# Kernel optimization log

Hardware: AMD Instinct MI355X
Metric: run time of the kernel (lower is better)

Reference implementation:

```python
import jax, jax.numpy as jnp
import numpy as np

B, K, N, E, D = 32, 32, 2048, 16384, 768
L_GNN, L_TR, H = 2, 4, 12
FF, VOCAB, N_ROLES, MAX_POS, N_HOPS = 3072, 25, 2, 64, 16


def setup_inputs() -> dict:
    key = jax.random.key(0)
    ks = jax.random.split(key, 32)
    s = 0.02
    inp = {
        "raw_features": jax.random.normal(ks[0], (B, K, D), jnp.float32),
        "x0": jax.random.randint(ks[1], (K, N), 0, VOCAB),
        "edge0": jax.random.randint(ks[2], (K, 2, E), 0, N),
        "batch0": jnp.sort(jax.random.randint(ks[3], (K, N), 0, B), axis=-1),
        "x1": jax.random.randint(ks[4], (K, N), 0, VOCAB),
        "edge1": jax.random.randint(ks[5], (K, 2, E), 0, N),
        "batch1": jnp.sort(jax.random.randint(ks[6], (K, N), 0, B), axis=-1),
        "role_ids": jax.random.randint(ks[7], (B, K), 0, N_ROLES),
        "position_ids": jax.random.randint(ks[8], (B, K), 0, MAX_POS),
        "hop_ids": jax.random.randint(ks[9], (B, K), 0, N_HOPS),
        # GNNForProtein params (shared across slots and both proteins)
        "amino_embed": jax.random.normal(ks[10], (VOCAB, D)) * s,
        "gnn_W": jax.random.normal(ks[11], (L_GNN, D, D)) * s,
        "gnn_b": jnp.zeros((L_GNN, D)),
        # GraphBert embeddings
        "role_emb": jax.random.normal(ks[12], (N_ROLES, D)) * s,
        "pos_emb": jax.random.normal(ks[13], (MAX_POS, D)) * s,
        "hop_emb": jax.random.normal(ks[14], (N_HOPS, D)) * s,
        "emb_ln_scale": jnp.ones((D,)),
        "emb_ln_bias": jnp.zeros((D,)),
        # GraphBert transformer layers (stacked over L_TR)
        "Wq": jax.random.normal(ks[15], (L_TR, D, D)) * s,
        "bq": jnp.zeros((L_TR, D)),
        "Wk": jax.random.normal(ks[16], (L_TR, D, D)) * s,
        "bk": jnp.zeros((L_TR, D)),
        "Wv": jax.random.normal(ks[17], (L_TR, D, D)) * s,
        "bv": jnp.zeros((L_TR, D)),
        "Wo": jax.random.normal(ks[18], (L_TR, D, D)) * s,
        "bo": jnp.zeros((L_TR, D)),
        "ln1_s": jnp.ones((L_TR, D)),
        "ln1_b": jnp.zeros((L_TR, D)),
        "W1": jax.random.normal(ks[19], (L_TR, D, FF)) * s,
        "b1": jnp.zeros((L_TR, FF)),
        "W2": jax.random.normal(ks[20], (L_TR, FF, D)) * s,
        "b2": jnp.zeros((L_TR, D)),
        "ln2_s": jnp.ones((L_TR, D)),
        "ln2_b": jnp.zeros((L_TR, D)),
    }
    return inp


def _ln(x, s, b):
    m = jnp.mean(x, -1, keepdims=True)
    v = jnp.mean(jnp.square(x - m), -1, keepdims=True)
    return (x - m) * jax.lax.rsqrt(v + 1e-12) * s + b


def _gnn(node_ids, edges, batch_idx, amino_embed, W, b):
    # One protein slot: GCN message passing + mean readout per graph in batch.
    h = amino_embed[node_ids]                      # [N, D]
    src, dst = edges[0], edges[1]
    for l in range(W.shape[0]):
        agg = jax.ops.segment_sum(h[src], dst, num_segments=N)
        h = jax.nn.relu((h + agg) @ W[l] + b[l])
    sums = jax.ops.segment_sum(h, batch_idx, num_segments=B)
    cnt = jax.ops.segment_sum(jnp.ones((h.shape[0], 1), h.dtype), batch_idx, num_segments=B)
    return sums / jnp.maximum(cnt, 1.0)           # [B, D]


def reference(raw_features, x0, edge0, batch0, x1, edge1, batch1, role_ids, position_ids, hop_ids,
              amino_embed, gnn_W, gnn_b, role_emb, pos_emb, hop_emb, emb_ln_scale, emb_ln_bias,
              Wq, bq, Wk, bk, Wv, bv, Wo, bo, ln1_s, ln1_b, W1, b1, W2, b2, ln2_s, ln2_b):
    # vmap over the K protein slots replaces the original Python loop (same math).
    gnn_v = jax.vmap(_gnn, in_axes=(0, 0, 0, None, None, None))
    p0 = gnn_v(x0, edge0, batch0, amino_embed, gnn_W, gnn_b)   # [K, B, D]
    p1 = gnn_v(x1, edge1, batch1, amino_embed, gnn_W, gnn_b)   # [K, B, D]
    feats = raw_features + jnp.transpose(p0 + p1, (1, 0, 2))   # [B, K, D]
    # GraphBert embeddings + encoder
    h = feats + role_emb[role_ids] + pos_emb[position_ids] + hop_emb[hop_ids]
    h = _ln(h, emb_ln_scale, emb_ln_bias)
    dh = D // H
    scale = float(1.0 / np.sqrt(dh))
    for l in range(Wq.shape[0]):
        q = (h @ Wq[l] + bq[l]).reshape(B, K, H, dh)
        kk = (h @ Wk[l] + bk[l]).reshape(B, K, H, dh)
        v = (h @ Wv[l] + bv[l]).reshape(B, K, H, dh)
        att = jax.nn.softmax(jnp.einsum('bqhd,bkhd->bhqk', q, kk) * scale, axis=-1)
        ctx = jnp.einsum('bhqk,bkhd->bqhd', att, v).reshape(B, K, D)
        h = _ln(h + ctx @ Wo[l] + bo[l], ln1_s[l], ln1_b[l])
        f = jax.nn.gelu(h @ W1[l] + b1[l]) @ W2[l] + b2[l]
        h = _ln(h + f, ln2_s[l], ln2_b[l])
    return h
```

## Files before the change

kernel.cpp:

```cpp
#include <hip/hip_runtime.h>
#include <hip/hip_bf16.h>
#include <math.h>

using bf16 = __hip_bfloat16;
typedef __attribute__((ext_vector_type(8))) short short8;
typedef __attribute__((ext_vector_type(4))) float floatx4;
typedef __attribute__((ext_vector_type(4))) short short4v;

#define NB   32
#define NK   32
#define NNODE 2048
#define NEDGE 16384
#define ND   768
#define NHH  12
#define DHH  64
#define NFF  3072
#define NG   64
#define LTR  4
#define VOCAB 25

static __device__ __forceinline__ float b2f(bf16 x) { return __bfloat162float(x); }
static __device__ __forceinline__ bf16 f2b(float x) { return __float2bfloat16(x); }
static __device__ __forceinline__ float bs2f(short s) {
    unsigned u = ((unsigned)(unsigned short)s) << 16;
    float f; __builtin_memcpy(&f, &u, 4); return f;
}
static __device__ __forceinline__ short f2bs(float x) {
    bf16 h = f2b(x); short s; __builtin_memcpy(&s, &h, 2); return s;
}

static __device__ __forceinline__ void load_lds16(const bf16* g, bf16* l) {
    __builtin_amdgcn_global_load_lds((const __attribute__((address_space(1))) void*)g,
                                     (__attribute__((address_space(3))) void*)l, 16, 0, 0);
}

static __device__ __forceinline__ float ldf(const void* p, size_t i, bool f32) {
    return f32 ? ((const float*)p)[i] : b2f(((const bf16*)p)[i]);
}

__global__ void detect_dtype_kernel(const void* __restrict__ eln_s, int* __restrict__ flag) {
    if (threadIdx.x == 0 && blockIdx.x == 0) {
        unsigned w = ((const unsigned*)eln_s)[0];
        flag[0] = (w == 0x3F800000u) ? 1 : 0;
    }
}

__device__ __forceinline__ void conv_tile(const void* __restrict__ src, size_t srcOff,
                                          bf16* __restrict__ dst, int R, int Cn,
                                          int tr, int tc, bool f32, int t,
                                          short (*tile)[70]) {
    int r0 = tr * 64, c0 = tc * 64;
    int rr = t >> 4, c4 = (t & 15) * 4;
    #pragma unroll
    for (int p = 0; p < 4; ++p) {
        int r = rr + p * 16;
        size_t base = srcOff + (size_t)(r0 + r) * Cn + c0 + c4;
        short4v s;
        if (f32) {
            float4 v = *(const float4*)((const float*)src + base);
            s.x = f2bs(v.x); s.y = f2bs(v.y); s.z = f2bs(v.z); s.w = f2bs(v.w);
        } else {
            s = *(const short4v*)((const short*)src + base);
        }
        tile[r][c4]     = s.x; tile[r][c4 + 1] = s.y;
        tile[r][c4 + 2] = s.z; tile[r][c4 + 3] = s.w;
    }
    __syncthreads();
    #pragma unroll
    for (int p = 0; p < 4; ++p) {
        int c = rr + p * 16;
        short4v o;
        o.x = tile[c4][c];     o.y = tile[c4 + 1][c];
        o.z = tile[c4 + 2][c]; o.w = tile[c4 + 3][c];
        *(short4v*)((short*)dst + (size_t)(c0 + c) * R + r0 + c4) = o;
    }
}

__global__ __launch_bounds__(256) void convert_gnn_kernel(const void* __restrict__ gnnW,
                                                          bf16* __restrict__ gnnT,
                                                          const int* __restrict__ flag) {
    __shared__ short tile[64][70];
    bool f32 = flag[0] != 0;
    int bid = blockIdx.x;
    int id = bid / 144, tl = bid % 144;
    conv_tile(gnnW, (size_t)id * 589824, gnnT + (size_t)id * 589824,
              768, 768, tl / 12, tl % 12, f32, threadIdx.x, tile);
}

__global__ __launch_bounds__(256) void convert_layer_kernel(
    const void* __restrict__ Wq, const void* __restrict__ Wk, const void* __restrict__ Wv,
    const void* __restrict__ Wo, const void* __restrict__ W1, const void* __restrict__ W2,
    int l, bf16* __restrict__ qkvT, bf16* __restrict__ oT,
    bf16* __restrict__ w1T, bf16* __restrict__ w2T, const int* __restrict__ flag) {
    __shared__ short tile[64][70];
    bool f32 = flag[0] != 0;
    int bid = blockIdx.x, t = threadIdx.x;
    if (bid < 432) {
        int m = bid / 144, tl = bid % 144;
        const void* src = (m == 0) ? Wq : ((m == 1) ? Wk : Wv);
        conv_tile(src, (size_t)l * 589824, qkvT + (size_t)m * 589824,
                  768, 768, tl / 12, tl % 12, f32, t, tile);
    } else if (bid < 576) {
        int tl = bid - 432;
        conv_tile(Wo, (size_t)l * 589824, oT, 768, 768, tl / 12, tl % 12, f32, t, tile);
    } else if (bid < 1152) {
        int tl = bid - 576;
        conv_tile(W1, (size_t)l * 768 * 3072, w1T, 768, 3072, tl / 48, tl % 48, f32, t, tile);
    } else {
        int tl = bid - 1152;
        conv_tile(W2, (size_t)l * 3072 * 768, w2T, 3072, 768, tl / 12, tl % 12, f32, t, tile);
    }
}

__global__ __launch_bounds__(256) void pack_bias_kernel(
    const void* __restrict__ gnnb, const void* __restrict__ bq, const void* __restrict__ bk,
    const void* __restrict__ bv, const void* __restrict__ bo, const void* __restrict__ b1,
    const void* __restrict__ b2, float* __restrict__ out, const int* __restrict__ flag) {
    bool f32 = flag[0] != 0;
    int i = blockIdx.x * 256 + threadIdx.x;
    if (i >= 1536 + LTR * 6912) return;
    float v;
    if (i < 1536) v = ldf(gnnb, i, f32);
    else {
        int j = i - 1536, l = j / 6912, r = j % 6912;
        if      (r <  768) v = ldf(bq, l * 768 + r, f32);
        else if (r < 1536) v = ldf(bk, l * 768 + r - 768, f32);
        else if (r < 2304) v = ldf(bv, l * 768 + r - 1536, f32);
        else if (r < 3072) v = ldf(bo, l * 768 + r - 2304, f32);
        else if (r < 6144) v = ldf(b1, l * 3072 + r - 3072, f32);
        else               v = ldf(b2, l * 768 + r - 6144, f32);
    }
    out[i] = v;
}

__global__ __launch_bounds__(192) void e1_kernel(const void* __restrict__ emb,
                                                 const bf16* __restrict__ w0T,
                                                 bf16* __restrict__ E1,
                                                 const int* __restrict__ flag) {
    bool f32 = flag[0] != 0;
    int v = blockIdx.x, t = threadIdx.x;
    float acc[4] = {0.f, 0.f, 0.f, 0.f};
    for (int k = 0; k < ND; k += 4) {
        float e0 = ldf(emb, (size_t)v * ND + k,     f32);
        float e1 = ldf(emb, (size_t)v * ND + k + 1, f32);
        float e2 = ldf(emb, (size_t)v * ND + k + 2, f32);
        float e3 = ldf(emb, (size_t)v * ND + k + 3, f32);
        #pragma unroll
        for (int j = 0; j < 4; ++j) {
            const short4v w = *(const short4v*)&w0T[(size_t)(t * 4 + j) * ND + k];
            acc[j] += e0 * bs2f(w.x) + e1 * bs2f(w.y) + e2 * bs2f(w.z) + e3 * bs2f(w.w);
        }
    }
    short4v o; o.x = f2bs(acc[0]); o.y = f2bs(acc[1]); o.z = f2bs(acc[2]); o.w = f2bs(acc[3]);
    ((short4v*)(E1 + (size_t)v * ND))[t] = o;
}

__global__ __launch_bounds__(256) void count_deg_kernel(const int* __restrict__ edge0,
                                                        const int* __restrict__ edge1,
                                                        int* __restrict__ deg) {
    int gid = blockIdx.x;
    int g = gid >> 6, chunk = gid & 63;
    const int* ep = (g < NK) ? (edge0 + (size_t)g * 2 * NEDGE)
                             : (edge1 + (size_t)(g - NK) * 2 * NEDGE);
    int e = chunk * 256 + threadIdx.x;
    int dst = ep[NEDGE + e];
    atomicAdd(&deg[g * NNODE + dst], 1);
}

__global__ __launch_bounds__(256) void scan_deg_kernel(int* __restrict__ deg,
                                                       int* __restrict__ indptr) {
    int g = blockIdx.x, t = threadIdx.x;
    __shared__ int sums[256];
    int loc[8]; int s = 0;
    #pragma unroll
    for (int i = 0; i < 8; ++i) { loc[i] = deg[g * NNODE + t * 8 + i]; s += loc[i]; }
    sums[t] = s; __syncthreads();
    for (int off = 1; off < 256; off <<= 1) {
        int v = (t >= off) ? sums[t - off] : 0;
        __syncthreads();
        sums[t] += v;
        __syncthreads();
    }
    int run = sums[t] - s;
    #pragma unroll
    for (int i = 0; i < 8; ++i) {
        indptr[g * (NNODE + 1) + t * 8 + i] = run;
        deg[g * NNODE + t * 8 + i] = run;
        run += loc[i];
    }
    if (t == 255) indptr[g * (NNODE + 1) + NNODE] = run;
}

__global__ __launch_bounds__(256) void fill_csr_kernel(const int* __restrict__ edge0,
                                                       const int* __restrict__ edge1,
                                                       int* __restrict__ cursor,
                                                       int* __restrict__ csr_src) {
    int gid = blockIdx.x;
    int g = gid >> 6, chunk = gid & 63;
    const int* ep = (g < NK) ? (edge0 + (size_t)g * 2 * NEDGE)
                             : (edge1 + (size_t)(g - NK) * 2 * NEDGE);
    int e = chunk * 256 + threadIdx.x;
    int src = ep[e];
    int dst = ep[NEDGE + e];
    int p = atomicAdd(&cursor[g * NNODE + dst], 1);
    csr_src[(size_t)g * NEDGE + p] = src;
}

__global__ __launch_bounds__(64) void batch_count_kernel(const int* __restrict__ batch0,
                                                         const int* __restrict__ batch1,
                                                         int* __restrict__ cnt) {
    int g = blockIdx.x;
    int b = threadIdx.x;
    if (b >= NB) return;
    const int* bp = (g < NK) ? (batch0 + (size_t)g * NNODE)
                             : (batch1 + (size_t)(g - NK) * NNODE);
    int lo = 0, hi = NNODE;
    while (lo < hi) { int mid = (lo + hi) >> 1; if (bp[mid] < b) lo = mid + 1; else hi = mid; }
    int start = lo;
    hi = NNODE;
    while (lo < hi) { int mid = (lo + hi) >> 1; if (bp[mid] < b + 1) lo = mid + 1; else hi = mid; }
    cnt[g * NB + b] = lo - start;
}

static __device__ __forceinline__ void node_block_decode(int id, int& gl, int& n) {
    int r = id & 7, q = id >> 3;
    gl = r + 8 * (q >> 11);
    n = q & 2047;
}

__global__ __launch_bounds__(192) void gnn_layer1_kernel(const int* __restrict__ x0,
                                                         const int* __restrict__ x1,
                                                         const bf16* __restrict__ E1,
                                                         const float* __restrict__ b0,
                                                         const int* __restrict__ indptr,
                                                         const int* __restrict__ csr_src,
                                                         bf16* __restrict__ hC, int g0) {
    int gl, n; node_block_decode(blockIdx.x, gl, n);
    int g = g0 + gl;
    const int* xg = (g < NK) ? (x0 + (size_t)g * NNODE) : (x1 + (size_t)(g - NK) * NNODE);
    int beg = indptr[g * (NNODE + 1) + n];
    int end = indptr[g * (NNODE + 1) + n + 1];
    const int* cs = csr_src + (size_t)g * NEDGE;
    int t = threadIdx.x;
    const short4v* E = (const short4v*)E1;
    short4v v = E[(size_t)xg[n] * 192 + t];
    float a0 = bs2f(v.x), a1 = bs2f(v.y), a2 = bs2f(v.z), a3 = bs2f(v.w);
    for (int e = beg; e < end; ++e) {
        int s = cs[e];
        short4v w = E[(size_t)xg[s] * 192 + t];
        a0 += bs2f(w.x); a1 += bs2f(w.y); a2 += bs2f(w.z); a3 += bs2f(w.w);
    }
    float4 bb = ((const float4*)b0)[t];
    short4v o;
    o.x = f2bs(fmaxf(a0 + bb.x, 0.f));
    o.y = f2bs(fmaxf(a1 + bb.y, 0.f));
    o.z = f2bs(fmaxf(a2 + bb.z, 0.f));
    o.w = f2bs(fmaxf(a3 + bb.w, 0.f));
    ((short4v*)(hC + ((size_t)gl * NNODE + n) * ND))[t] = o;
}

__global__ __launch_bounds__(192) void gnn_aggregate_kernel(const bf16* __restrict__ hC,
                                                            const int* __restrict__ indptr,
                                                            const int* __restrict__ csr_src,
                                                            bf16* __restrict__ xC, int g0) {
    int gl, n; node_block_decode(blockIdx.x, gl, n);
    int g = g0 + gl;
    int beg = indptr[g * (NNODE + 1) + n];
    int end = indptr[g * (NNODE + 1) + n + 1];
    const short4v* hg = (const short4v*)(hC + (size_t)gl * NNODE * ND);
    const int* cs = csr_src + (size_t)g * NEDGE;
    int t = threadIdx.x;
    short4v v = hg[(size_t)n * 192 + t];
    float a0 = bs2f(v.x), a1 = bs2f(v.y), a2 = bs2f(v.z), a3 = bs2f(v.w);
    for (int e = beg; e < end; ++e) {
        int s = cs[e];
        short4v w = hg[(size_t)s * 192 + t];
        a0 += bs2f(w.x); a1 += bs2f(w.y); a2 += bs2f(w.z); a3 += bs2f(w.w);
    }
    short4v o; o.x = f2bs(a0); o.y = f2bs(a1); o.z = f2bs(a2); o.w = f2bs(a3);
    ((short4v*)(xC + ((size_t)gl * NNODE + n) * ND))[t] = o;
}

__global__ __launch_bounds__(256) void gemm_tn(const bf16* __restrict__ A,
                                               const bf16* __restrict__ BT,
                                               const float* __restrict__ bias,
                                               void* __restrict__ C,
                                               int M, int K, int N,
                                               int act, int outF32,
                                               const int* __restrict__ batAp,
                                               const int* __restrict__ batBp,
                                               float* __restrict__ pool, int g0) {
    __shared__ bf16 lA[2][128][32];
    __shared__ bf16 lB[2][128][32];
    int nTilesN = N >> 7, nTilesM = M >> 7;
    int brow, bcol;
    if ((nTilesM & 7) == 0) {
        int xcd = blockIdx.x & 7, j = blockIdx.x >> 3;
        brow = (j / nTilesN) * 8 + xcd;
        bcol = j % nTilesN;
    } else {
        bcol = blockIdx.x % nTilesN;
        brow = blockIdx.x / nTilesN;
    }
    int t = threadIdx.x;
    int wave = t >> 6, lane = t & 63;
    int wr = wave >> 1, wc = wave & 1;
    int l15 = lane & 15, quad = lane >> 4;
    const int row0 = brow << 7, col0 = bcol << 7;
    const int sr0 = t >> 2, sk0 = (t & 3) * 8;
    const bf16* Ab = A + (size_t)(row0 + sr0) * K + sk0;
    const bf16* Bb = BT + (size_t)(col0 + sr0) * K + sk0;
    const size_t rstride = (size_t)64 * K;

    load_lds16(Ab,           &lA[0][sr0][sk0]);
    load_lds16(Ab + rstride, &lA[0][sr0 + 64][sk0]);
    load_lds16(Bb,           &lB[0][sr0][sk0]);
    load_lds16(Bb + rstride, &lB[0][sr0 + 64][sk0]);

    floatx4 acc[4][4] = {};
    int cur = 0;
    for (int k0 = 0; k0 < K; k0 += 32) {
        __syncthreads();
        if (k0 + 32 < K) {
            load_lds16(Ab + k0 + 32,           &lA[cur ^ 1][sr0][sk0]);
            load_lds16(Ab + rstride + k0 + 32, &lA[cur ^ 1][sr0 + 64][sk0]);
            load_lds16(Bb + k0 + 32,           &lB[cur ^ 1][sr0][sk0]);
            load_lds16(Bb + rstride + k0 + 32, &lB[cur ^ 1][sr0 + 64][sk0]);
        }
        short8 afr[4], bfr[4];
        #pragma unroll
        for (int i = 0; i < 4; ++i)
            afr[i] = *reinterpret_cast<const short8*>(&lA[cur][wr * 64 + i * 16 + l15][quad * 8]);
        #pragma unroll
        for (int j = 0; j < 4; ++j)
            bfr[j] = *reinterpret_cast<const short8*>(&lB[cur][wc * 64 + j * 16 + l15][quad * 8]);
        #pragma unroll
        for (int i = 0; i < 4; ++i)
            #pragma unroll
            for (int j = 0; j < 4; ++j)
                acc[i][j] = __builtin_amdgcn_mfma_f32_16x16x32_bf16(afr[i], bfr[j], acc[i][j], 0, 0, 0);
        cur ^= 1;
    }

    if (pool) {
        int g = g0 + (row0 >> 11);
        const int* bp = (g < NK) ? (batAp + (size_t)g * NNODE)
                                 : (batBp + (size_t)(g - NK) * NNODE);
        int nbase = row0 & (NNODE - 1);
        float* pg = pool + (size_t)g * NB * ND;
        int cb = wc * 64 + l15;
        float bv[4];
        #pragma unroll
        for (int j = 0; j < 4; ++j) bv[j] = bias[col0 + cb + j * 16];
        __syncthreads();
        float* lp = (float*)lA;
        int bLo = bp[nbase], bHi = bp[nbase + 127];
        int nb = (bHi - bLo + 1) * 128;
        for (int idx = t; idx < nb; idx += 256) lp[idx] = 0.f;
        __syncthreads();
        float sums[4] = {0.f, 0.f, 0.f, 0.f};
        int curb = -1;
        #pragma unroll
        for (int i = 0; i < 4; ++i) {
            int rr = nbase + wr * 64 + i * 16 + quad * 4;
            #pragma unroll
            for (int r = 0; r < 4; ++r) {
                int b = bp[rr + r];
                if (b != curb) {
                    if (curb >= 0) {
                        #pragma unroll
                        for (int j = 0; j < 4; ++j)
                            atomicAdd(&lp[(curb - bLo) * 128 + cb + j * 16], sums[j]);
                    }
                    curb = b;
                    sums[0] = sums[1] = sums[2] = sums[3] = 0.f;
                }
                #pragma unroll
                for (int j = 0; j < 4; ++j) {
                    float v = acc[i][j][r] + bv[j];
                    if (act == 1) v = fmaxf(v, 0.f);
                    sums[j] += v;
                }
            }
        }
        #pragma unroll
        for (int j = 0; j < 4; ++j)
            atomicAdd(&lp[(curb - bLo) * 128 + cb + j * 16], sums[j]);
        __syncthreads();
        for (int idx = t; idx < nb; idx += 256) {
            float v = lp[idx];
            if (v != 0.f)
                atomicAdd(&pg[(size_t)(bLo + (idx >> 7)) * ND + col0 + (idx & 127)], v);
        }
        return;
    }

    #pragma unroll
    for (int i = 0; i < 4; ++i) {
        int rbase = row0 + wr * 64 + i * 16 + quad * 4;
        #pragma unroll
        for (int j = 0; j < 4; ++j) {
            int c = col0 + wc * 64 + j * 16 + l15;
            float bv = bias[c];
            #pragma unroll
            for (int r = 0; r < 4; ++r) {
                float v = acc[i][j][r] + bv;
                if (act == 1) v = fmaxf(v, 0.f);
                else if (act == 2) {
                    float x = v;
                    float u = 1.5957691216057308f * (x + 0.044715f * x * x * x);
                    v = x / (1.f + __expf(-u));
                }
                size_t idx = (size_t)(rbase + r) * N + c;
                if (outF32) ((float*)C)[idx] = v;
                else        ((bf16*)C)[idx] = f2b(v);
            }
        }
    }
}

__global__ __launch_bounds__(256) void gemm_tn_sk(const bf16* __restrict__ A,
                                                  const bf16* __restrict__ BT,
                                                  const float* __restrict__ bias,
                                                  void* __restrict__ C,
                                                  int M, int K, int N, int splitK,
                                                  int act, int store) {
    __shared__ bf16 lA[2][64][32];
    __shared__ bf16 lB[2][128][32];
    int nTilesN = N >> 7, nTilesM = M >> 6;
    int tiles = nTilesM * nTilesN;
    int split = blockIdx.x / tiles;
    int jt = blockIdx.x % tiles;
    int brow = jt / nTilesN, bcol = jt % nTilesN;
    int t = threadIdx.x;
    int wave = t >> 6, lane = t & 63;
    int wr = wave >> 1, wc = wave & 1;
    int l15 = lane & 15, quad = lane >> 4;
    const int row0 = brow << 6, col0 = bcol << 7;
    const int kLen = K / splitK, kBeg = split * kLen;
    const int sr0 = t >> 2, sk0 = (t & 3) * 8;
    const bf16* Ab = A + (size_t)(row0 + sr0) * K + kBeg + sk0;
    const bf16* Bb = BT + (size_t)(col0 + sr0) * K + kBeg + sk0;
    const size_t rstride = (size_t)64 * K;

    load_lds16(Ab,           &lA[0][sr0][sk0]);
    load_lds16(Bb,           &lB[0][sr0][sk0]);
    load_lds16(Bb + rstride, &lB[0][sr0 + 64][sk0]);

    floatx4 acc[2][4] = {};
    int cur = 0;
    for (int k0 = 0; k0 < kLen; k0 += 32) {
        __syncthreads();
        if (k0 + 32 < kLen) {
            load_lds16(Ab + k0 + 32,           &lA[cur ^ 1][sr0][sk0]);
            load_lds16(Bb + k0 + 32,           &lB[cur ^ 1][sr0][sk0]);
            load_lds16(Bb + rstride + k0 + 32, &lB[cur ^ 1][sr0 + 64][sk0]);
        }
        short8 afr[2], bfr[4];
        #pragma unroll
        for (int i = 0; i < 2; ++i)
            afr[i] = *reinterpret_cast<const short8*>(&lA[cur][wr * 32 + i * 16 + l15][quad * 8]);
        #pragma unroll
        for (int j = 0; j < 4; ++j)
            bfr[j] = *reinterpret_cast<const short8*>(&lB[cur][wc * 64 + j * 16 + l15][quad * 8]);
        #pragma unroll
        for (int i = 0; i < 2; ++i)
            #pragma unroll
            for (int j = 0; j < 4; ++j)
                acc[i][j] = __builtin_amdgcn_mfma_f32_16x16x32_bf16(afr[i], bfr[j], acc[i][j], 0, 0, 0);
        cur ^= 1;
    }
    #pragma unroll
    for (int i = 0; i < 2; ++i) {
        int rbase = row0 + wr * 32 + i * 16 + quad * 4;
        #pragma unroll
        for (int j = 0; j < 4; ++j) {
            int c = col0 + wc * 64 + j * 16 + l15;
            float bv = (split == 0) ? bias[c] : 0.f;
            #pragma unroll
            for (int r = 0; r < 4; ++r) {
                float v = acc[i][j][r] + bv;
                if (act == 1) v = fmaxf(v, 0.f);
                else if (act == 2) {
                    float x = v;
                    float u = 1.5957691216057308f * (x + 0.044715f * x * x * x);
                    v = x / (1.f + __expf(-u));
                }
                size_t idx = (size_t)(rbase + r) * N + c;
                if (store == 0)      atomicAdd(&((float*)C)[idx], v);
                else if (store == 1) ((float*)C)[idx] = v;
                else                 ((bf16*)C)[idx] = f2b(v);
            }
        }
    }
}

__device__ __forceinline__ void block_ln_768(float (&x)[3], int t,
                                             const void* __restrict__ s,
                                             const void* __restrict__ b,
                                             size_t sOff, bool f32,
                                             float (&y)[3], float* red) {
    float loc = x[0] + x[1] + x[2];
    red[t] = loc; __syncthreads();
    for (int off = 128; off > 0; off >>= 1) {
        if (t < off) red[t] += red[t + off];
        __syncthreads();
    }
    float mean = red[0] * (1.f / 768.f);
    __syncthreads();
    float vs = 0.f;
    #pragma unroll
    for (int e = 0; e < 3; ++e) { float d = x[e] - mean; vs += d * d; }
    red[t] = vs; __syncthreads();
    for (int off = 128; off > 0; off >>= 1) {
        if (t < off) red[t] += red[t + off];
        __syncthreads();
    }
    float var = red[0] * (1.f / 768.f);
    __syncthreads();
    float inv = rsqrtf(var + 1e-12f);
    #pragma unroll
    for (int e = 0; e < 3; ++e) {
        int d = t + e * 256;
        y[e] = (x[e] - mean) * inv * ldf(s, sOff + d, f32) + ldf(b, sOff + d, f32);
    }
}

__global__ __launch_bounds__(256) void combine_embed_ln_kernel(
    const void* __restrict__ raw, const float* __restrict__ pooled,
    const int* __restrict__ cnt,
    const int* __restrict__ role_ids, const int* __restrict__ pos_ids, const int* __restrict__ hop_ids,
    const void* __restrict__ role_emb, const void* __restrict__ pos_emb, const void* __restrict__ hop_emb,
    const void* __restrict__ lns, const void* __restrict__ lnb,
    float* __restrict__ hT, bf16* __restrict__ hbf,
    const int* __restrict__ flag) {
    bool f32 = flag[0] != 0;
    __shared__ float red[256];
    int token = blockIdx.x;
    int b = token >> 5, k = token & 31;
    int t = threadIdx.x;
    int rid = role_ids[b * NK + k];
    int pid = pos_ids[b * NK + k];
    int hid = hop_ids[b * NK + k];
    float inv0 = 1.f / (float)max(cnt[k * NB + b], 1);
    float inv1 = 1.f / (float)max(cnt[(NK + k) * NB + b], 1);
    float x[3], y[3];
    #pragma unroll
    for (int e = 0; e < 3; ++e) {
        int d = t + e * 256;
        float p0 = pooled[((size_t)k * NB + b) * ND + d] * inv0;
        float p1 = pooled[((size_t)(NK + k) * NB + b) * ND + d] * inv1;
        x[e] = ldf(raw, (size_t)token * ND + d, f32) + p0 + p1
             + ldf(role_emb, (size_t)rid * ND + d, f32)
             + ldf(pos_emb, (size_t)pid * ND + d, f32)
             + ldf(hop_emb, (size_t)hid * ND + d, f32);
    }
    block_ln_768(x, t, lns, lnb, 0, f32, y, red);
    #pragma unroll
    for (int e = 0; e < 3; ++e) {
        int d = t + e * 256;
        hT[(size_t)token * ND + d] = y[e];
        hbf[(size_t)token * ND + d] = f2b(y[e]);
    }
}

__global__ __launch_bounds__(256) void add_ln_kernel(float* __restrict__ hT,
                                                     const void* __restrict__ lns,
                                                     const void* __restrict__ lnb,
                                                     unsigned long long sOff,
                                                     void* __restrict__ outp, int extOut,
                                                     const int* __restrict__ flag) {
    bool f32 = flag[0] != 0;
    __shared__ float red[256];
    int token = blockIdx.x;
    int t = threadIdx.x;
    float x[3], y[3];
    #pragma unroll
    for (int e = 0; e < 3; ++e) {
        int d = t + e * 256;
        x[e] = hT[(size_t)token * ND + d];
    }
    block_ln_768(x, t, lns, lnb, sOff, f32, y, red);
    #pragma unroll
    for (int e = 0; e < 3; ++e) {
        int d = t + e * 256;
        size_t idx = (size_t)token * ND + d;
        hT[idx] = y[e];
        if (extOut && f32) ((float*)outp)[idx] = y[e];
        else               ((bf16*)outp)[idx] = f2b(y[e]);
    }
}

__global__ __launch_bounds__(256) void attn_kernel(const bf16* __restrict__ qkv,
                                                   bf16* __restrict__ ctx) {
    int blk = blockIdx.x;
    int b = blk / NHH, h = blk % NHH;
    __shared__ float lq[NK][DHH], lk[NK][DHH], lv[NK][DHH];
    __shared__ float ls[NK][NK];
    int t = threadIdx.x;
    {
        int tok = t >> 3, d8 = (t & 7) * 8;
        size_t base = ((size_t)(b * NK + tok)) * (3 * ND) + h * DHH + d8;
        short8 q8 = *(const short8*)&qkv[base];
        short8 k8 = *(const short8*)&qkv[base + ND];
        short8 v8 = *(const short8*)&qkv[base + 2 * ND];
        #pragma unroll
        for (int j = 0; j < 8; ++j) {
            lq[tok][d8 + j] = bs2f(q8[j]);
            lk[tok][d8 + j] = bs2f(k8[j]);
            lv[tok][d8 + j] = bs2f(v8[j]);
        }
    }
    __syncthreads();
    const float scale = 0.125f;
    for (int i = t; i < NK * NK; i += 256) {
        int qi = i >> 5, kj = i & 31;
        float s = 0.f;
        #pragma unroll
        for (int d = 0; d < DHH; ++d) s += lq[qi][d] * lk[kj][d];
        ls[qi][kj] = s * scale;
    }
    __syncthreads();
    if (t < NK) {
        float m = -1e30f;
        for (int j = 0; j < NK; ++j) m = fmaxf(m, ls[t][j]);
        float sum = 0.f;
        for (int j = 0; j < NK; ++j) { float e = expf(ls[t][j] - m); ls[t][j] = e; sum += e; }
        float inv = 1.f / sum;
        for (int j = 0; j < NK; ++j) ls[t][j] *= inv;
    }
    __syncthreads();
    for (int i = t; i < NK * DHH; i += 256) {
        int qi = i >> 6, d = i & 63;
        float s = 0.f;
        #pragma unroll
        for (int j = 0; j < NK; ++j) s += ls[qi][j] * lv[j][d];
        ctx[((size_t)(b * NK + qi)) * ND + h * DHH + d] = f2b(s);
    }
}

extern "C" void kernel_launch(void* const* d_in, const int* in_sizes, int n_in,
                              void* d_out, int out_size, void* d_ws, size_t ws_size,
                              hipStream_t stream) {
    const void* raw      = d_in[0];
    const int*  x0       = (const int*)d_in[1];
    const int*  edge0    = (const int*)d_in[2];
    const int*  batch0   = (const int*)d_in[3];
    const int*  x1       = (const int*)d_in[4];
    const int*  edge1    = (const int*)d_in[5];
    const int*  batch1   = (const int*)d_in[6];
    const int*  role_ids = (const int*)d_in[7];
    const int*  pos_ids  = (const int*)d_in[8];
    const int*  hop_ids  = (const int*)d_in[9];
    const void* amino    = d_in[10];
    const void* gnnW     = d_in[11];
    const void* gnnb     = d_in[12];
    const void* role_emb = d_in[13];
    const void* pos_emb  = d_in[14];
    const void* hop_emb  = d_in[15];
    const void* eln_s    = d_in[16];
    const void* eln_b    = d_in[17];
    const void* Wq       = d_in[18];
    const void* bq       = d_in[19];
    const void* Wk       = d_in[20];
    const void* bk       = d_in[21];
    const void* Wv       = d_in[22];
    const void* bv       = d_in[23];
    const void* Wo       = d_in[24];
    const void* bo       = d_in[25];
    const void* ln1_s    = d_in[26];
    const void* ln1_b    = d_in[27];
    const void* W1       = d_in[28];
    const void* b1       = d_in[29];
    const void* W2       = d_in[30];
    const void* b2       = d_in[31];
    const void* ln2_s    = d_in[32];
    const void* ln2_b    = d_in[33];

    char* ws = (char*)d_ws;
    size_t off = 0;
    auto alloc = [&](size_t bytes) -> void* {
        void* p = ws + off;
        off = (off + bytes + 255) & ~(size_t)255;
        return p;
    };
    int*   dflag   = (int*)alloc(256);
    float* pooled  = (float*)alloc((size_t)NG * NB * ND * 4);
    int*   cntb    = (int*)alloc((size_t)NG * NB * 4);
    int*   indptr  = (int*)alloc((size_t)NG * (NNODE + 1) * 4);
    int*   csr_src = (int*)alloc((size_t)NG * NEDGE * 4);
    int*   degcur  = (int*)alloc((size_t)NG * NNODE * 4);
    bf16*  gnnT    = (bf16*)alloc((size_t)2 * ND * ND * 2);
    bf16*  E1      = (bf16*)alloc((size_t)VOCAB * ND * 2);
    float* biasPk  = (float*)alloc((size_t)(1536 + LTR * 6912) * 4);
    const size_t QS = (size_t)3 * ND * ND, OS = (size_t)ND * ND;
    const size_t S1 = (size_t)ND * NFF,    S2 = (size_t)NFF * ND;
    bf16*  qkvT    = (bf16*)alloc(QS * 2);
    bf16*  oT      = (bf16*)alloc(OS * 2);
    bf16*  w1T     = (bf16*)alloc(S1 * 2);
    bf16*  w2T     = (bf16*)alloc(S2 * 2);

    const size_t perG  = (size_t)NNODE * ND * 2;
    const size_t bigTR = 21 * 1024 * 1024;
    int gc = 8;
    for (int cand = 32; cand >= 8; cand >>= 1) {
        size_t bigGNN = 2 * (size_t)cand * perG;
        size_t need = off + (bigGNN > bigTR ? bigGNN : bigTR) + (1 << 20);
        if (need <= ws_size) { gc = cand; break; }
    }
    char* bigbase = (char*)alloc(2 * (size_t)gc * perG > bigTR ? 2 * (size_t)gc * perG : bigTR);
    bf16* hC = (bf16*)bigbase;
    bf16* xC = (bf16*)(bigbase + (size_t)gc * perG);
    size_t toff = 0;
    auto talloc = [&](size_t bytes) -> void* {
        void* p = bigbase + toff;
        toff = (toff + bytes + 255) & ~(size_t)255;
        return p;
    };
    float* hT    = (float*)talloc((size_t)NB * NK * ND * 4);
    bf16*  hbf   = (bf16*)talloc((size_t)NB * NK * ND * 2);
    bf16*  qkvb  = (bf16*)talloc((size_t)NB * NK * 3 * ND * 2);
    bf16*  ctxb  = (bf16*)talloc((size_t)NB * NK * ND * 2);
    bf16*  ffbuf = (bf16*)talloc((size_t)NB * NK * NFF * 2);

    auto gemm_sk = [&](const bf16* A, const bf16* BT, const float* bias, void* C,
                       int Mm, int Kk, int Nn, int splitK, int act, int store) {
        int blocks = (Mm >> 6) * (Nn >> 7) * splitK;
        gemm_tn_sk<<<blocks, 256, 0, stream>>>(A, BT, bias, C, Mm, Kk, Nn, splitK, act, store);
    };

    detect_dtype_kernel<<<1, 64, 0, stream>>>(eln_s, dflag);

    convert_gnn_kernel<<<288, 256, 0, stream>>>(gnnW, gnnT, dflag);
    pack_bias_kernel<<<(1536 + LTR * 6912 + 255) / 256, 256, 0, stream>>>(
        gnnb, bq, bk, bv, bo, b1, b2, biasPk, dflag);
    e1_kernel<<<VOCAB, 192, 0, stream>>>(amino, gnnT, E1, dflag);

    hipMemsetAsync(degcur, 0, (size_t)NG * NNODE * 4, stream);
    hipMemsetAsync(pooled, 0, (size_t)NG * NB * ND * 4, stream);
    count_deg_kernel<<<NG * 64, 256, 0, stream>>>(edge0, edge1, degcur);
    scan_deg_kernel<<<NG, 256, 0, stream>>>(degcur, indptr);
    fill_csr_kernel<<<NG * 64, 256, 0, stream>>>(edge0, edge1, degcur, csr_src);
    batch_count_kernel<<<NG, 64, 0, stream>>>(batch0, batch1, cntb);

    for (int g0 = 0; g0 < NG; g0 += gc) {
        gnn_layer1_kernel<<<gc * NNODE, 192, 0, stream>>>(x0, x1, E1, biasPk,
                                                          indptr, csr_src, hC, g0);
        gnn_aggregate_kernel<<<gc * NNODE, 192, 0, stream>>>(hC, indptr, csr_src, xC, g0);
        int blocks = ((gc * NNODE) >> 7) * (ND >> 7);
        gemm_tn<<<blocks, 256, 0, stream>>>(xC, gnnT + (size_t)ND * ND, biasPk + ND, nullptr,
                                            gc * NNODE, ND, ND, 1, 0,
                                            batch0, batch1, pooled, g0);
    }

    combine_embed_ln_kernel<<<NB * NK, 256, 0, stream>>>(
        raw, pooled, cntb, role_ids, pos_ids, hop_ids,
        role_emb, pos_emb, hop_emb, eln_s, eln_b, hT, hbf, dflag);

    const int M = NB * NK;
    for (int l = 0; l < LTR; ++l) {
        convert_layer_kernel<<<1728, 256, 0, stream>>>(Wq, Wk, Wv, Wo, W1, W2, l,
                                                       qkvT, oT, w1T, w2T, dflag);
        const float* lb = biasPk + 1536 + l * 6912;
        gemm_sk(hbf, qkvT, lb, qkvb, M, ND, 3 * ND, 1, 0, 2);
        attn_kernel<<<NB * NHH, 256, 0, stream>>>(qkvb, ctxb);
        gemm_sk(ctxb, oT, lb + 2304, hT, M, ND, ND, 2, 0, 0);
        add_ln_kernel<<<M, 256, 0, stream>>>(hT, ln1_s, ln1_b,
                                             (unsigned long long)l * ND, hbf, 0, dflag);
        gemm_sk(hbf, w1T, lb + 3072, ffbuf, M, ND, NFF, 1, 2, 2);
        gemm_sk(ffbuf, w2T, lb + 6144, hT, M, NFF, ND, 4, 0, 0);
        int ext = (l == LTR - 1) ? 1 : 0;
        void* outb = ext ? d_out : (void*)hbf;
        add_ln_kernel<<<M, 256, 0, stream>>>(hT, ln2_s, ln2_b,
                                             (unsigned long long)l * ND, outb, ext, dflag);
    }
}
```

Measured before the change: 1.374 ms.

## Replace GNN pooling GEMM with 256x128 tile, 8-wave pipelined swizzled-LDS kernel

Result: no change. 1.373 ms (-0.1%).

```diff
diff --git a/kernel.cpp b/kernel.cpp
--- a/kernel.cpp
+++ b/kernel.cpp
@@ -281,141 +281,142 @@
     ((short4v*)(xC + ((size_t)gl * NNODE + n) * ND))[t] = o;
 }
 
-__global__ __launch_bounds__(256) void gemm_tn(const bf16* __restrict__ A,
-                                               const bf16* __restrict__ BT,
-                                               const float* __restrict__ bias,
-                                               void* __restrict__ C,
-                                               int M, int K, int N,
-                                               int act, int outF32,
-                                               const int* __restrict__ batAp,
-                                               const int* __restrict__ batBp,
-                                               float* __restrict__ pool, int g0) {
-    __shared__ bf16 lA[2][128][32];
-    __shared__ bf16 lB[2][128][32];
-    int nTilesN = N >> 7, nTilesM = M >> 7;
-    int brow, bcol;
-    if ((nTilesM & 7) == 0) {
-        int xcd = blockIdx.x & 7, j = blockIdx.x >> 3;
-        brow = (j / nTilesN) * 8 + xcd;
-        bcol = j % nTilesN;
-    } else {
-        bcol = blockIdx.x % nTilesN;
-        brow = blockIdx.x / nTilesN;
-    }
+__global__ __launch_bounds__(512) void gemm8_pool(const bf16* __restrict__ A,
+                                                  const bf16* __restrict__ BT,
+                                                  const float* __restrict__ bias,
+                                                  int M, int K, int N,
+                                                  const int* __restrict__ batAp,
+                                                  const int* __restrict__ batBp,
+                                                  float* __restrict__ pool, int g0) {
+    __shared__ bf16 sA[3][256][64];
+    __shared__ bf16 sB[2][128][64];
+    const int nt = K >> 6;
+    int nTN = N >> 7;
+    int xcd = blockIdx.x & 7, jb = blockIdx.x >> 3;
+    int brow = (jb / nTN) * 8 + xcd;
+    int bcol = jb % nTN;
+    const int row0 = brow << 8, col0 = bcol << 7;
     int t = threadIdx.x;
-    int wave = t >> 6, lane = t & 63;
-    int wr = wave >> 1, wc = wave & 1;
-    int l15 = lane & 15, quad = lane >> 4;
-    const int row0 = brow << 7, col0 = bcol << 7;
-    const int sr0 = t >> 2, sk0 = (t & 3) * 8;
-    const bf16* Ab = A + (size_t)(row0 + sr0) * K + sk0;
-    const bf16* Bb = BT + (size_t)(col0 + sr0) * K + sk0;
-    const size_t rstride = (size_t)64 * K;
-
-    load_lds16(Ab,           &lA[0][sr0][sk0]);
-    load_lds16(Ab + rstride, &lA[0][sr0 + 64][sk0]);
-    load_lds16(Bb,           &lB[0][sr0][sk0]);
-    load_lds16(Bb + rstride, &lB[0][sr0 + 64][sk0]);
+    int wid = t >> 6, lane = t & 63;
+    int wr = wid >> 1, wc = wid & 1;
+    int l15 = lane & 15, kx = lane >> 4, sw = lane & 7;
+
+    const bf16* Abase = A + (size_t)row0 * K;
+    const bf16* Bbase = BT + (size_t)col0 * K;
+
+    auto stage = [&](const bf16* g, bf16* slot, int r0) {
+        int r = r0 + (t >> 3);
+        int ks = ((t & 7) ^ ((t >> 3) & 7)) << 3;
+        load_lds16(g + (size_t)r * K + ks, slot + ((size_t)r0 << 6) + ((size_t)t << 3));
+    };
+    auto rdA = [&](int s, int i, int kh) {
+        return *(const short8*)&sA[s][wr * 64 + i * 16 + l15][(((kh << 2) | kx) ^ sw) << 3];
+    };
+    auto rdB = [&](int s, int j, int kh) {
+        return *(const short8*)&sB[s][wc * 64 + j * 16 + l15][(((kh << 2) | kx) ^ sw) << 3];
+    };
+
+    stage(Abase, &sA[0][0][0], 0);   stage(Abase, &sA[0][0][0], 64);
+    stage(Abase, &sA[0][0][0], 128); stage(Abase, &sA[0][0][0], 192);
+    stage(Bbase, &sB[0][0][0], 0);   stage(Bbase, &sB[0][0][0], 64);
+    const bf16* gA1 = Abase + 64;
+    stage(gA1, &sA[1][0][0], 0);   stage(gA1, &sA[1][0][0], 64);
+    stage(gA1, &sA[1][0][0], 128); stage(gA1, &sA[1][0][0], 192);
+    asm volatile("s_waitcnt vmcnt(4)" ::: "memory");
+    __builtin_amdgcn_s_barrier();
 
     floatx4 acc[4][4] = {};
-    int cur = 0;
-    for (int k0 = 0; k0 < K; k0 += 32) {
-        __syncthreads();
-        if (k0 + 32 < K) {
-            load_lds16(Ab + k0 + 32,           &lA[cur ^ 1][sr0][sk0]);
-            load_lds16(Ab + rstride + k0 + 32, &lA[cur ^ 1][sr0 + 64][sk0]);
-            load_lds16(Bb + k0 + 32,           &lB[cur ^ 1][sr0][sk0]);
-            load_lds16(Bb + rstride + k0 + 32, &lB[cur ^ 1][sr0 + 64][sk0]);
+    for (int kt = 0; kt < nt; ++kt) {
+        int sa = kt % 3, sb = kt & 1;
+        bf16* saN = &sA[(kt + 2) % 3][0][0];
+        const bf16* gA = Abase + (kt + 2) * 64;
+        short8 af[4], bf[4];
+        #pragma unroll
+        for (int i = 0; i < 4; ++i) af[i] = rdA(sa, i, 0);
+        #pragma unroll
+        for (int j = 0; j < 4; ++j) bf[j] = rdB(sb, j, 0);
+        if (kt + 1 < nt) {
+            const bf16* gB = Bbase + (kt + 1) * 64;
+            bf16* sbN = &sB[(kt + 1) & 1][0][0];
+            stage(gB, sbN, 0); stage(gB, sbN, 64);
         }
-        short8 afr[4], bfr[4];
-        #pragma unroll
-        for (int i = 0; i < 4; ++i)
-            afr[i] = *reinterpret_cast<const short8*>(&lA[cur][wr * 64 + i * 16 + l15][quad * 8]);
-        #pragma unroll
-        for (int j = 0; j < 4; ++j)
-            bfr[j] = *reinterpret_cast<const short8*>(&lB[cur][wc * 64 + j * 16 + l15][quad * 8]);
+        if (kt + 2 < nt) { stage(gA, saN, 0); stage(gA, saN, 64); }
+        __builtin_amdgcn_s_barrier();
+        asm volatile("s_waitcnt lgkmcnt(0)" ::: "memory");
+        __builtin_amdgcn_s_setprio(1);
         #pragma unroll
         for (int i = 0; i < 4; ++i)
             #pragma unroll
             for (int j = 0; j < 4; ++j)
-                acc[i][j] = __builtin_amdgcn_mfma_f32_16x16x32_bf16(afr[i], bfr[j], acc[i][j], 0, 0, 0);
-        cur ^= 1;
-    }
-
-    if (pool) {
-        int g = g0 + (row0 >> 11);
-        const int* bp = (g < NK) ? (batAp + (size_t)g * NNODE)
-                                 : (batBp + (size_t)(g - NK) * NNODE);
-        int nbase = row0 & (NNODE - 1);
-        float* pg = pool + (size_t)g * NB * ND;
-        int cb = wc * 64 + l15;
-        float bv[4];
-        #pragma unroll
-        for (int j = 0; j < 4; ++j) bv[j] = bias[col0 + cb + j * 16];
-        __syncthreads();
-        float* lp = (float*)lA;
-        int bLo = bp[nbase], bHi = bp[nbase + 127];
-        int nb = (bHi - bLo + 1) * 128;
-        for (int idx = t; idx < nb; idx += 256) lp[idx] = 0.f;
-        __syncthreads();
-        float sums[4] = {0.f, 0.f, 0.f, 0.f};
-        int curb = -1;
-        #pragma unroll
-        for (int i = 0; i < 4; ++i) {
-            int rr = nbase + wr * 64 + i * 16 + quad * 4;
+                acc[i][j] = __builtin_amdgcn_mfma_f32_16x16x32_bf16(af[i], bf[j], acc[i][j], 0, 0, 0);
+        __builtin_amdgcn_s_setprio(0);
+        __builtin_amdgcn_s_barrier();
+        #pragma unroll
+        for (int i = 0; i < 4; ++i) af[i] = rdA(sa, i, 1);
+        #pragma unroll
+        for (int j = 0; j < 4; ++j) bf[j] = rdB(sb, j, 1);
+        if (kt + 2 < nt) { stage(gA, saN, 128); stage(gA, saN, 192); }
+        __builtin_amdgcn_s_barrier();
+        asm volatile("s_waitcnt lgkmcnt(0)" ::: "memory");
+        __builtin_amdgcn_s_setprio(1);
+        #pragma unroll
+        for (int i = 0; i < 4; ++i)
             #pragma unroll
-            for (int r = 0; r < 4; ++r) {
-                int b = bp[rr + r];
-                if (b != curb) {
-                    if (curb >= 0) {
-                        #pragma unroll
-                        for (int j = 0; j < 4; ++j)
-                            atomicAdd(&lp[(curb - bLo) * 128 + cb + j * 16], sums[j]);
-                    }
-                    curb = b;
-                    sums[0] = sums[1] = sums[2] = sums[3] = 0.f;
+            for (int j = 0; j < 4; ++j)
+                acc[i][j] = __builtin_amdgcn_mfma_f32_16x16x32_bf16(af[i], bf[j], acc[i][j], 0, 0, 0);
+        __builtin_amdgcn_s_setprio(0);
+        if (kt + 1 < nt) {
+            if (kt + 2 < nt) asm volatile("s_waitcnt vmcnt(4)" ::: "memory");
+            else             asm volatile("s_waitcnt vmcnt(0)" ::: "memory");
+            __builtin_amdgcn_s_barrier();
+        }
+    }
+
+    __syncthreads();
+    int g = g0 + (row0 >> 11);
+    const int* bp = (g < NK) ? (batAp + (size_t)g * NNODE)
+                             : (batBp + (size_t)(g - NK) * NNODE);
+    int nbase = row0 & (NNODE - 1);
+    float* pg = pool + (size_t)g * NB * ND;
+    int cb = wc * 64 + l15;
+    float bv[4];
+    #pragma unroll
+    for (int j = 0; j < 4; ++j) bv[j] = bias[col0 + cb + j * 16];
+    float* lp = (float*)sA;
+    int bLo = bp[nbase], bHi = bp[nbase + 255];
+    int nb = (bHi - bLo + 1) * 128;
+    for (int idx = t; idx < nb; idx += 512) lp[idx] = 0.f;
+    __syncthreads();
+    float sums[4] = {0.f, 0.f, 0.f, 0.f};
+    int curb = -1;
+    #pragma unroll
+    for (int i = 0; i < 4; ++i) {
+        int rr = nbase + wr * 64 + i * 16 + kx * 4;
+        #pragma unroll
+        for (int r = 0; r < 4; ++r) {
+            int b = bp[rr + r];
+            if (b != curb) {
+                if (curb >= 0) {
+                    #pragma unroll
+                    for (int j = 0; j < 4; ++j)
+                        atomicAdd(&lp[(curb - bLo) * 128 + cb + j * 16], sums[j]);
                 }
-                #pragma unroll
-                for (int j = 0; j < 4; ++j) {
-                    float v = acc[i][j][r] + bv[j];
-                    if (act == 1) v = fmaxf(v, 0.f);
-                    sums[j] += v;
-                }
+                curb = b;
+                sums[0] = sums[1] = sums[2] = sums[3] = 0.f;
             }
+            #pragma unroll
+            for (int j = 0; j < 4; ++j)
+                sums[j] += fmaxf(acc[i][j][r] + bv[j], 0.f);
         }
-        #pragma unroll
-        for (int j = 0; j < 4; ++j)
-            atomicAdd(&lp[(curb - bLo) * 128 + cb + j * 16], sums[j]);
-        __syncthreads();
-        for (int idx = t; idx < nb; idx += 256) {
-            float v = lp[idx];
-            if (v != 0.f)
-                atomicAdd(&pg[(size_t)(bLo + (idx >> 7)) * ND + col0 + (idx & 127)], v);
-        }
-        return;
-    }
-
-    #pragma unroll
-    for (int i = 0; i < 4; ++i) {
-        int rbase = row0 + wr * 64 + i * 16 + quad * 4;
-        #pragma unroll
-        for (int j = 0; j < 4; ++j) {
-            int c = col0 + wc * 64 + j * 16 + l15;
-            float bv = bias[c];
-            #pragma unroll
-            for (int r = 0; r < 4; ++r) {
-                float v = acc[i][j][r] + bv;
-                if (act == 1) v = fmaxf(v, 0.f);
-                else if (act == 2) {
-                    float x = v;
-                    float u = 1.5957691216057308f * (x + 0.044715f * x * x * x);
-                    v = x / (1.f + __expf(-u));
-                }
-                size_t idx = (size_t)(rbase + r) * N + c;
-                if (outF32) ((float*)C)[idx] = v;
-                else        ((bf16*)C)[idx] = f2b(v);
-            }
-        }
+    }
+    #pragma unroll
+    for (int j = 0; j < 4; ++j)
+        atomicAdd(&lp[(curb - bLo) * 128 + cb + j * 16], sums[j]);
+    __syncthreads();
+    for (int idx = t; idx < nb; idx += 512) {
+        float v = lp[idx];
+        if (v != 0.f)
+            atomicAdd(&pg[(size_t)(bLo + (idx >> 7)) * ND + col0 + (idx & 127)], v);
     }
 }
 
@@ -747,10 +748,10 @@
         gnn_layer1_kernel<<<gc * NNODE, 192, 0, stream>>>(x0, x1, E1, biasPk,
                                                           indptr, csr_src, hC, g0);
         gnn_aggregate_kernel<<<gc * NNODE, 192, 0, stream>>>(hC, indptr, csr_src, xC, g0);
-        int blocks = ((gc * NNODE) >> 7) * (ND >> 7);
-        gemm_tn<<<blocks, 256, 0, stream>>>(xC, gnnT + (size_t)ND * ND, biasPk + ND, nullptr,
-                                            gc * NNODE, ND, ND, 1, 0,
-                                            batch0, batch1, pooled, g0);
+        int blocks = ((gc * NNODE) >> 8) * (ND >> 7);
+        gemm8_pool<<<blocks, 512, 0, stream>>>(xC, gnnT + (size_t)ND * ND, biasPk + ND,
+                                               gc * NNODE, ND, ND,
+                                               batch0, batch1, pooled, g0);
     }
 
     combine_embed_ln_kernel<<<NB * NK, 256, 0, stream>>>(
```
